# Performance work log

Measured on AMD Instinct MI355X. Metric: run time of the kernel, lower is better.

The kernel has to match this reference:

```python
import jax, jax.numpy as jnp
import numpy as np

CHANNEL = 512
INTER = CHANNEL // 2


def setup_inputs() -> dict:
    key = jax.random.key(0)
    k0, k1, k2, k3, k4 = jax.random.split(key, 5)
    b, c, h, w = 8, CHANNEL, 64, 64
    x = jax.random.normal(k0, (b, c, h, w), dtype=jnp.float32)
    # 1x1 conv weights, no bias: (out_ch, in_ch)
    s_in = 1.0 / np.sqrt(c)
    s_inter = 1.0 / np.sqrt(INTER)
    w_phi = jax.random.uniform(k1, (INTER, c), jnp.float32, -s_in, s_in)
    w_theta = jax.random.uniform(k2, (INTER, c), jnp.float32, -s_in, s_in)
    w_g = jax.random.uniform(k3, (INTER, c), jnp.float32, -s_in, s_in)
    w_mask = jax.random.uniform(k4, (c, INTER), jnp.float32, -s_inter, s_inter)
    return {"x": x, "w_phi": w_phi, "w_theta": w_theta, "w_g": w_g, "w_mask": w_mask}


def reference(x, w_phi, w_theta, w_g, w_mask):
    b, c, h, w = x.shape
    inter = c // 2
    # NOTE: original torch code views the (b, inter, h, w) conv outputs as
    # (b, c, -1), so n = h*w // 2 and the matmul 'feature' dim is the full c.
    n = (h * w) // 2
    phi = jnp.einsum('oc,bchw->bohw', w_phi, x).reshape(b, c, n)        # (b, c, n)
    theta = jnp.einsum('oc,bchw->bohw', w_theta, x).reshape(b, c, n)
    theta = jnp.transpose(theta, (0, 2, 1))                              # (b, n, c)
    g = jnp.einsum('oc,bchw->bohw', w_g, x).reshape(b, c, n)
    g = jnp.transpose(g, (0, 2, 1))                                      # (b, n, c)
    attn = jnp.matmul(theta, phi)                                        # (b, n, n)
    attn = jax.nn.softmax(attn, axis=1)                                  # softmax over dim=1 (columns)
    y = jnp.matmul(attn, g)                                              # (b, n, c)
    y = jnp.transpose(y, (0, 2, 1)).reshape(b, inter, h, w)              # (b, inter, h, w)
    mask = jnp.einsum('oc,bchw->bohw', w_mask, y)                        # (b, c, h, w)
    return mask + x
```

## Files before the change

### kernel.cpp

```cpp
#include <hip/hip_runtime.h>
#include <cstdint>
#include <cstddef>

typedef __attribute__((ext_vector_type(8))) _Float16 half8;
typedef __attribute__((ext_vector_type(4))) float floatx4;

static __device__ __forceinline__ uint16_t f2h(float f) {
    _Float16 h = (_Float16)f;
    uint16_t u;
    __builtin_memcpy(&u, &h, 2);
    return u;
}
static __device__ __forceinline__ float h2f(uint16_t u) {
    _Float16 h;
    __builtin_memcpy(&h, &u, 2);
    return (float)h;
}

static __device__ __forceinline__ void g2lds16(const void* g, void* l) {
    __builtin_amdgcn_global_load_lds((__attribute__((address_space(1))) void*)g,
                                     (__attribute__((address_space(3))) void*)l, 16, 0, 0);
}

__global__ void cvt_weights(const float* __restrict__ wphi, const float* __restrict__ wtheta,
                            const float* __restrict__ wg, const float* __restrict__ wmask,
                            uint16_t* __restrict__ W3, uint16_t* __restrict__ Wm, float* __restrict__ L) {
    int seg = blockIdx.y;
    int i = blockIdx.x * 256 + threadIdx.x;
    if (seg == 4) {
        if (i < 16384) L[i] = 0.f;
        return;
    }
    const float* src = seg == 0 ? wphi : seg == 1 ? wtheta : seg == 2 ? wg : wmask;
    uint16_t* dst = seg < 3 ? W3 + seg * 131072 : Wm;
    int base = i * 4;
    float4 v = *(const float4*)(src + base);
    *(ushort4*)(dst + base) = make_ushort4(f2h(v.x), f2h(v.y), f2h(v.z), f2h(v.w));
}

__global__ void recip_f32(const float* __restrict__ l, float* __restrict__ r) {
    int i = blockIdx.x * 256 + threadIdx.x;
    r[i] = 1.f / l[i];
}

__global__ __launch_bounds__(256) void transpose_x(const float* __restrict__ x, uint16_t* __restrict__ xt) {
    __shared__ uint16_t tile[64][66];
    int b = blockIdx.z, p0 = blockIdx.x * 64, c0 = blockIdx.y * 64;
    int t0 = threadIdx.x & 63, t1 = threadIdx.x >> 6;
    const float* xb = x + ((long)b * 512 + c0) * 4096 + p0;
#pragma unroll
    for (int r = 0; r < 16; ++r) {
        int cc = t1 * 16 + r;
        tile[cc][t0] = f2h(xb[(long)cc * 4096 + t0]);
    }
    __syncthreads();
    uint16_t* xtb = xt + ((long)b * 4096 + p0) * 512 + c0;
#pragma unroll
    for (int r = 0; r < 16; ++r) {
        int pp = t1 * 16 + r;
        xtb[(long)pp * 512 + t0] = tile[t0][pp];
    }
}

template <bool KHALF, int EPI, bool SWAP, bool ASOFT, bool BGATHER>
__global__ __launch_bounds__(256) void gemm_nt(const uint16_t* __restrict__ A, const uint16_t* __restrict__ B,
                                               void* __restrict__ Cout, const float* __restrict__ resid,
                                               int lda, int ldb, int ldc, int nK,
                                               long aBatch, long bBatch, long cBatch,
                                               void* __restrict__ Cout2, int ldc2, long c2Batch,
                                               float* __restrict__ Lsum, const float* __restrict__ Rvec) {
    __shared__ uint16_t Al[128 * 32];
    __shared__ uint16_t Bl[128 * 32];
    const int b = blockIdx.z;
    const uint16_t* Ab = A + (long)b * aBatch;
    const uint16_t* Bb = B + (long)b * bBatch;
    const int m0 = (SWAP ? blockIdx.y : blockIdx.x) * 128;
    const int n0 = (SWAP ? blockIdx.x : blockIdx.y) * 128;
    const int tid = threadIdx.x;
    const int lane = tid & 63, wave = tid >> 6;
    const int ln = lane & 15, q = lane >> 4;
    const int wm = (wave & 1) * 64, wn = (wave >> 1) * 64;

    floatx4 acc[4][4];
#pragma unroll
    for (int i = 0; i < 4; ++i)
#pragma unroll
        for (int j = 0; j < 4; ++j) acc[i][j] = (floatx4){0.f, 0.f, 0.f, 0.f};

    for (int kt = 0; kt < nK; ++kt) {
        int k0 = kt * 32;
        int keff = k0;
        long roff = 0;
        if (KHALF && k0 >= 256) { keff = k0 - 256; roff = 2048; }
#pragma unroll
        for (int s = 0; s < 2; ++s) {
            int c = tid + s * 256;
            int row = c >> 2, kq = (c & 3) * 8;
            if (ASOFT) {
                uint4 v = *(const uint4*)(Ab + (long)(m0 + row) * lda + keff + kq);
                const float* Rp = Rvec + (long)b * 2048 + keff + kq;
                float4 ra = *(const float4*)Rp;
                float4 rb = *(const float4*)(Rp + 4);
                float rr[8] = {ra.x, ra.y, ra.z, ra.w, rb.x, rb.y, rb.z, rb.w};
                uint32_t* pv = (uint32_t*)&v;
                uint32_t o[4];
#pragma unroll
                for (int e = 0; e < 4; ++e) {
                    float va = h2f((uint16_t)(pv[e] & 0xffffu));
                    float vb = h2f((uint16_t)(pv[e] >> 16));
                    float pa = __expf(va - 12.f) * rr[2 * e];
                    float pb = __expf(vb - 12.f) * rr[2 * e + 1];
                    o[e] = (uint32_t)f2h(pa) | ((uint32_t)f2h(pb) << 16);
                }
                *(uint4*)&Al[c * 8] = *(uint4*)o;
            } else {
                g2lds16(Ab + ((long)(m0 + row) + roff) * lda + keff + kq, &Al[c * 8]);
            }
            if (BGATHER) {
                int pg = n0 + row;
                int ii = pg & 2047, hh = pg >> 11;
                const uint16_t* src = Bb + (long)ii * 512 + 2 * (keff + kq);
                uint4 v0 = *(const uint4*)src;
                uint4 v1 = *(const uint4*)(src + 8);
                uint32_t* a = (uint32_t*)&v0;
                uint32_t* cc = (uint32_t*)&v1;
                uint32_t o[4];
                if (hh == 0) {
                    o[0] = (a[0] & 0xffffu) | (a[1] << 16);
                    o[1] = (a[2] & 0xffffu) | (a[3] << 16);
                    o[2] = (cc[0] & 0xffffu) | (cc[1] << 16);
                    o[3] = (cc[2] & 0xffffu) | (cc[3] << 16);
                } else {
                    o[0] = (a[0] >> 16) | (a[1] & 0xffff0000u);
                    o[1] = (a[2] >> 16) | (a[3] & 0xffff0000u);
                    o[2] = (cc[0] >> 16) | (cc[1] & 0xffff0000u);
                    o[3] = (cc[2] >> 16) | (cc[3] & 0xffff0000u);
                }
                *(uint4*)&Bl[c * 8] = *(uint4*)o;
            } else {
                g2lds16(Bb + ((long)(n0 + row) + roff) * ldb + keff + kq, &Bl[c * 8]);
            }
        }
        __syncthreads();
        half8 af[4], bfr[4];
#pragma unroll
        for (int mt = 0; mt < 4; ++mt) af[mt] = *(const half8*)&Al[(wm + mt * 16 + ln) * 32 + q * 8];
#pragma unroll
        for (int nt = 0; nt < 4; ++nt) bfr[nt] = *(const half8*)&Bl[(wn + nt * 16 + ln) * 32 + q * 8];
#pragma unroll
        for (int mt = 0; mt < 4; ++mt)
#pragma unroll
            for (int nt = 0; nt < 4; ++nt)
                acc[mt][nt] = __builtin_amdgcn_mfma_f32_16x16x32_f16(af[mt], bfr[nt], acc[mt][nt], 0, 0, 0);
        __syncthreads();
    }

    if (EPI == 0 || (EPI == 3 && n0 < 512)) {
        uint16_t* C = (uint16_t*)Cout + (long)b * cBatch;
#pragma unroll
        for (int mt = 0; mt < 4; ++mt)
#pragma unroll
            for (int r = 0; r < 4; ++r) {
                int gm = m0 + wm + mt * 16 + q * 4 + r;
#pragma unroll
                for (int nt = 0; nt < 4; ++nt) {
                    int gn = n0 + wn + nt * 16 + ln;
                    C[(long)gm * ldc + gn] = f2h(acc[mt][nt][r]);
                }
            }
    } else if (EPI == 4) {
        uint16_t* C = (uint16_t*)Cout + (long)b * cBatch;
        float cs[4] = {0.f, 0.f, 0.f, 0.f};
#pragma unroll
        for (int mt = 0; mt < 4; ++mt)
#pragma unroll
            for (int r = 0; r < 4; ++r) {
                int gm = m0 + wm + mt * 16 + q * 4 + r;
#pragma unroll
                for (int nt = 0; nt < 4; ++nt) {
                    int gn = n0 + wn + nt * 16 + ln;
                    uint16_t hh = f2h(acc[mt][nt][r]);
                    C[(long)gm * ldc + gn] = hh;
                    cs[nt] += __expf(h2f(hh) - 12.f);
                }
            }
#pragma unroll
        for (int nt = 0; nt < 4; ++nt) {
            float s = cs[nt];
            s += __shfl_xor(s, 16);
            s += __shfl_xor(s, 32);
            if (q == 0) atomicAdd(&Lsum[(long)b * 2048 + n0 + wn + nt * 16 + ln], s);
        }
    } else if (EPI == 1) {
        float* C = (float*)Cout + (long)b * cBatch;
        const float* X = resid + (long)b * cBatch;
#pragma unroll
        for (int mt = 0; mt < 4; ++mt)
#pragma unroll
            for (int r = 0; r < 4; ++r) {
                int gm = m0 + wm + mt * 16 + q * 4 + r;
#pragma unroll
                for (int nt = 0; nt < 4; ++nt) {
                    int gn = n0 + wn + nt * 16 + ln;
                    long idx = (long)gm * ldc + gn;
                    C[idx] = acc[mt][nt][r] + X[idx];
                }
            }
    } else {
        uint16_t* C = (uint16_t*)Cout2 + (long)b * c2Batch;
#pragma unroll
        for (int nt = 0; nt < 4; ++nt) {
            int gn2 = n0 - 512 + wn + nt * 16 + ln;
#pragma unroll
            for (int mt = 0; mt < 4; ++mt) {
                int gmB = m0 + wm + mt * 16 + q * 4;
                ushort4 u = make_ushort4(f2h(acc[mt][nt][0]), f2h(acc[mt][nt][1]), f2h(acc[mt][nt][2]),
                                         f2h(acc[mt][nt][3]));
                *(ushort4*)&C[(long)gn2 * ldc2 + gmB] = u;
            }
        }
    }
}

extern "C" void kernel_launch(void* const* d_in, const int* in_sizes, int n_in, void* d_out, int out_size, void* d_ws,
                              size_t ws_size, hipStream_t stream) {
    const float* x = (const float*)d_in[0];
    const float* wphi = (const float*)d_in[1];
    const float* wtheta = (const float*)d_in[2];
    const float* wg = (const float*)d_in[3];
    const float* wmask = (const float*)d_in[4];
    float* out = (float*)d_out;
    char* ws = (char*)d_ws;

    uint16_t* W3 = (uint16_t*)(ws + 0);
    uint16_t* Wm = (uint16_t*)(ws + 786432);
    float* L = (float*)(ws + 1048576);
    float* R = (float*)(ws + 1114112);
    char* A_region = ws + 1179648;
    char* B_region = ws + 68288512;
    uint16_t* Xt = (uint16_t*)A_region;
    uint16_t* S = (uint16_t*)A_region;
    uint16_t* C2 = (uint16_t*)B_region;
    uint16_t* Y2 = (uint16_t*)B_region;
    uint16_t* Gc = (uint16_t*)(B_region + 33554432);

    cvt_weights<<<dim3(128, 5), 256, 0, stream>>>(wphi, wtheta, wg, wmask, W3, Wm, L);

    transpose_x<<<dim3(64, 8, 8), 256, 0, stream>>>(x, Xt);

    gemm_nt<false, 3, false, false, false><<<dim3(32, 6, 8), 256, 0, stream>>>(
        Xt, W3, C2, nullptr, 512, 512, 512, 16, 4096L * 512, 0, 4096L * 512, Gc, 4096, 256L * 4096, nullptr, nullptr);

    gemm_nt<true, 4, false, false, false><<<dim3(16, 16, 8), 256, 0, stream>>>(
        C2 + 256, C2, S, nullptr, 512, 512, 2048, 16, 4096L * 512, 4096L * 512, 2048L * 2048, nullptr, 0, 0, L,
        nullptr);

    recip_f32<<<64, 256, 0, stream>>>(L, R);

    gemm_nt<false, 0, true, true, false><<<dim3(4, 16, 8), 256, 0, stream>>>(
        S, Gc, Y2, nullptr, 2048, 2048, 512, 64, 2048L * 2048, 1048576L, 2048L * 512, nullptr, 0, 0, nullptr, R);

    gemm_nt<false, 1, false, false, true><<<dim3(4, 32, 8), 256, 0, stream>>>(
        Wm, Y2, out, x, 256, 512, 4096, 8, 0, 1048576L, 512L * 4096, nullptr, 0, 0, nullptr, nullptr);
}
```

Before: 346.6 us.

## Store exp scores as bf16 and fold softmax normalization into G

The score GEMM epilogue now computes the exponential directly and stores it as bf16 probabilities-numerators. The per-column 1/L normalization moves from the A-load of the attention-times-G GEMM onto G via a small scale_g kernel, since scaling along the shared k dimension is equivalent. The PV GEMM then uses plain async global-to-LDS loads and bf16 MFMA instead of per-element exp and multiply in the load path. The cost is an extra pass over G and bf16 precision for P and scaled G.

Measured after the change: 319.2 us. 1.09x faster.

```diff
diff --git a/kernel.cpp b/kernel.cpp
--- a/kernel.cpp
+++ b/kernel.cpp
@@ -3,6 +3,7 @@
 #include <cstddef>
 
 typedef __attribute__((ext_vector_type(8))) _Float16 half8;
+typedef __attribute__((ext_vector_type(8))) short short8;
 typedef __attribute__((ext_vector_type(4))) float floatx4;
 
 static __device__ __forceinline__ uint16_t f2h(float f) {
@@ -15,6 +16,12 @@
     _Float16 h;
     __builtin_memcpy(&h, &u, 2);
     return (float)h;
+}
+static __device__ __forceinline__ uint16_t f2bf(float f) {
+    uint32_t u;
+    __builtin_memcpy(&u, &f, 4);
+    u += 0x7fffu + ((u >> 16) & 1u);
+    return (uint16_t)(u >> 16);
 }
 
 static __device__ __forceinline__ void g2lds16(const void* g, void* l) {
@@ -38,11 +45,6 @@
     *(ushort4*)(dst + base) = make_ushort4(f2h(v.x), f2h(v.y), f2h(v.z), f2h(v.w));
 }
 
-__global__ void recip_f32(const float* __restrict__ l, float* __restrict__ r) {
-    int i = blockIdx.x * 256 + threadIdx.x;
-    r[i] = 1.f / l[i];
-}
-
 __global__ __launch_bounds__(256) void transpose_x(const float* __restrict__ x, uint16_t* __restrict__ xt) {
     __shared__ uint16_t tile[64][66];
     int b = blockIdx.z, p0 = blockIdx.x * 64, c0 = blockIdx.y * 64;
@@ -62,13 +64,34 @@
     }
 }
 
-template <bool KHALF, int EPI, bool SWAP, bool ASOFT, bool BGATHER>
+__global__ void scale_g(uint16_t* __restrict__ gc, const float* __restrict__ L) {
+    long t = (long)blockIdx.x * 256 + threadIdx.x;
+    long base = t * 8;
+    int j0 = (int)(base & 2047);
+    int b = (int)(base >> 20);
+    const float* Lp = L + (long)b * 2048 + j0;
+    float4 l0 = *(const float4*)Lp;
+    float4 l1 = *(const float4*)(Lp + 4);
+    float rr[8] = {1.f / l0.x, 1.f / l0.y, 1.f / l0.z, 1.f / l0.w, 1.f / l1.x, 1.f / l1.y, 1.f / l1.z, 1.f / l1.w};
+    uint4 v = *(uint4*)(gc + base);
+    uint32_t* pv = (uint32_t*)&v;
+    uint32_t o[4];
+#pragma unroll
+    for (int e = 0; e < 4; ++e) {
+        float a = h2f((uint16_t)(pv[e] & 0xffffu)) * rr[2 * e];
+        float c = h2f((uint16_t)(pv[e] >> 16)) * rr[2 * e + 1];
+        o[e] = (uint32_t)f2bf(a) | ((uint32_t)f2bf(c) << 16);
+    }
+    *(uint4*)(gc + base) = *(uint4*)o;
+}
+
+template <bool KHALF, int EPI, bool SWAP, bool BGATHER, int DT>
 __global__ __launch_bounds__(256) void gemm_nt(const uint16_t* __restrict__ A, const uint16_t* __restrict__ B,
                                                void* __restrict__ Cout, const float* __restrict__ resid,
                                                int lda, int ldb, int ldc, int nK,
                                                long aBatch, long bBatch, long cBatch,
                                                void* __restrict__ Cout2, int ldc2, long c2Batch,
-                                               float* __restrict__ Lsum, const float* __restrict__ Rvec) {
+                                               float* __restrict__ Lsum) {
     __shared__ uint16_t Al[128 * 32];
     __shared__ uint16_t Bl[128 * 32];
     const int b = blockIdx.z;
@@ -96,26 +119,7 @@
         for (int s = 0; s < 2; ++s) {
             int c = tid + s * 256;
             int row = c >> 2, kq = (c & 3) * 8;
-            if (ASOFT) {
-                uint4 v = *(const uint4*)(Ab + (long)(m0 + row) * lda + keff + kq);
-                const float* Rp = Rvec + (long)b * 2048 + keff + kq;
-                float4 ra = *(const float4*)Rp;
-                float4 rb = *(const float4*)(Rp + 4);
-                float rr[8] = {ra.x, ra.y, ra.z, ra.w, rb.x, rb.y, rb.z, rb.w};
-                uint32_t* pv = (uint32_t*)&v;
-                uint32_t o[4];
-#pragma unroll
-                for (int e = 0; e < 4; ++e) {
-                    float va = h2f((uint16_t)(pv[e] & 0xffffu));
-                    float vb = h2f((uint16_t)(pv[e] >> 16));
-                    float pa = __expf(va - 12.f) * rr[2 * e];
-                    float pb = __expf(vb - 12.f) * rr[2 * e + 1];
-                    o[e] = (uint32_t)f2h(pa) | ((uint32_t)f2h(pb) << 16);
-                }
-                *(uint4*)&Al[c * 8] = *(uint4*)o;
-            } else {
-                g2lds16(Ab + ((long)(m0 + row) + roff) * lda + keff + kq, &Al[c * 8]);
-            }
+            g2lds16(Ab + ((long)(m0 + row) + roff) * lda + keff + kq, &Al[c * 8]);
             if (BGATHER) {
                 int pg = n0 + row;
                 int ii = pg & 2047, hh = pg >> 11;
@@ -142,16 +146,24 @@
             }
         }
         __syncthreads();
-        half8 af[4], bfr[4];
-#pragma unroll
-        for (int mt = 0; mt < 4; ++mt) af[mt] = *(const half8*)&Al[(wm + mt * 16 + ln) * 32 + q * 8];
-#pragma unroll
-        for (int nt = 0; nt < 4; ++nt) bfr[nt] = *(const half8*)&Bl[(wn + nt * 16 + ln) * 32 + q * 8];
-#pragma unroll
-        for (int mt = 0; mt < 4; ++mt)
-#pragma unroll
-            for (int nt = 0; nt < 4; ++nt)
-                acc[mt][nt] = __builtin_amdgcn_mfma_f32_16x16x32_f16(af[mt], bfr[nt], acc[mt][nt], 0, 0, 0);
+        short8 af[4], bfr[4];
+#pragma unroll
+        for (int mt = 0; mt < 4; ++mt) af[mt] = *(const short8*)&Al[(wm + mt * 16 + ln) * 32 + q * 8];
+#pragma unroll
+        for (int nt = 0; nt < 4; ++nt) bfr[nt] = *(const short8*)&Bl[(wn + nt * 16 + ln) * 32 + q * 8];
+#pragma unroll
+        for (int mt = 0; mt < 4; ++mt)
+#pragma unroll
+            for (int nt = 0; nt < 4; ++nt) {
+                if constexpr (DT == 0) {
+                    half8 ah, bh;
+                    __builtin_memcpy(&ah, &af[mt], 16);
+                    __builtin_memcpy(&bh, &bfr[nt], 16);
+                    acc[mt][nt] = __builtin_amdgcn_mfma_f32_16x16x32_f16(ah, bh, acc[mt][nt], 0, 0, 0);
+                } else {
+                    acc[mt][nt] = __builtin_amdgcn_mfma_f32_16x16x32_bf16(af[mt], bfr[nt], acc[mt][nt], 0, 0, 0);
+                }
+            }
         __syncthreads();
     }
 
@@ -179,9 +191,9 @@
 #pragma unroll
                 for (int nt = 0; nt < 4; ++nt) {
                     int gn = n0 + wn + nt * 16 + ln;
-                    uint16_t hh = f2h(acc[mt][nt][r]);
-                    C[(long)gm * ldc + gn] = hh;
-                    cs[nt] += __expf(h2f(hh) - 12.f);
+                    float e = __expf(acc[mt][nt][r] - 12.f);
+                    C[(long)gm * ldc + gn] = f2bf(e);
+                    cs[nt] += e;
                 }
             }
 #pragma unroll
@@ -235,11 +247,10 @@
     uint16_t* W3 = (uint16_t*)(ws + 0);
     uint16_t* Wm = (uint16_t*)(ws + 786432);
     float* L = (float*)(ws + 1048576);
-    float* R = (float*)(ws + 1114112);
     char* A_region = ws + 1179648;
     char* B_region = ws + 68288512;
     uint16_t* Xt = (uint16_t*)A_region;
-    uint16_t* S = (uint16_t*)A_region;
+    uint16_t* P = (uint16_t*)A_region;
     uint16_t* C2 = (uint16_t*)B_region;
     uint16_t* Y2 = (uint16_t*)B_region;
     uint16_t* Gc = (uint16_t*)(B_region + 33554432);
@@ -248,18 +259,17 @@
 
     transpose_x<<<dim3(64, 8, 8), 256, 0, stream>>>(x, Xt);
 
-    gemm_nt<false, 3, false, false, false><<<dim3(32, 6, 8), 256, 0, stream>>>(
-        Xt, W3, C2, nullptr, 512, 512, 512, 16, 4096L * 512, 0, 4096L * 512, Gc, 4096, 256L * 4096, nullptr, nullptr);
-
-    gemm_nt<true, 4, false, false, false><<<dim3(16, 16, 8), 256, 0, stream>>>(
-        C2 + 256, C2, S, nullptr, 512, 512, 2048, 16, 4096L * 512, 4096L * 512, 2048L * 2048, nullptr, 0, 0, L,
-        nullptr);
-
-    recip_f32<<<64, 256, 0, stream>>>(L, R);
-
-    gemm_nt<false, 0, true, true, false><<<dim3(4, 16, 8), 256, 0, stream>>>(
-        S, Gc, Y2, nullptr, 2048, 2048, 512, 64, 2048L * 2048, 1048576L, 2048L * 512, nullptr, 0, 0, nullptr, R);
-
-    gemm_nt<false, 1, false, false, true><<<dim3(4, 32, 8), 256, 0, stream>>>(
-        Wm, Y2, out, x, 256, 512, 4096, 8, 0, 1048576L, 512L * 4096, nullptr, 0, 0, nullptr, nullptr);
-}
+    gemm_nt<false, 3, false, false, 0><<<dim3(32, 6, 8), 256, 0, stream>>>(
+        Xt, W3, C2, nullptr, 512, 512, 512, 16, 4096L * 512, 0, 4096L * 512, Gc, 4096, 256L * 4096, nullptr);
+
+    gemm_nt<true, 4, false, false, 0><<<dim3(16, 16, 8), 256, 0, stream>>>(
+        C2 + 256, C2, P, nullptr, 512, 512, 2048, 16, 4096L * 512, 4096L * 512, 2048L * 2048, nullptr, 0, 0, L);
+
+    scale_g<<<4096, 256, 0, stream>>>(Gc, L);
+
+    gemm_nt<false, 0, true, false, 1><<<dim3(4, 16, 8), 256, 0, stream>>>(
+        P, Gc, Y2, nullptr, 2048, 2048, 512, 64, 2048L * 2048, 1048576L, 2048L * 512, nullptr, 0, 0, nullptr);
+
+    gemm_nt<false, 1, false, true, 0><<<dim3(4, 32, 8), 256, 0, stream>>>(
+        Wm, Y2, out, x, 256, 512, 4096, 8, 0, 1048576L, 512L * 4096, nullptr, 0, 0, nullptr);
+}
```
